# Kernel optimization log

Measured on AMD Instinct MI355X. Metric: run time of the kernel, lower is better.

Reference implementation:

```python
import jax, jax.numpy as jnp
import numpy as np

IN_C, H1, H2, FC1, NCLS = 16, 32, 64, 128, 10
N_NODES, N_EDGES = 20000, 100000


def _glorot(key, shape):
    fan_in, fan_out = shape[0], shape[-1]
    s = jnp.sqrt(6.0 / (fan_in + fan_out))
    return jax.random.uniform(key, shape, jnp.float32, -s, s)


def setup_inputs() -> dict:
    key = jax.random.key(0)
    ks = jax.random.split(key, 20)
    x = jax.random.normal(ks[0], (N_NODES, IN_C), jnp.float32)
    edge_index = jax.random.randint(ks[1], (2, N_EDGES), 0, N_NODES, jnp.int64)
    edge_attr = jax.random.uniform(ks[2], (N_EDGES, 1), jnp.float32)
    return {
        "x": x,
        "edge_index": edge_index,
        "edge_attr": edge_attr,
        # conv1 edge-MLP: 1 -> 25 -> IN_C*H1
        "w1a": _glorot(ks[3], (1, 25)), "b1a": jnp.zeros((25,), jnp.float32),
        "w1b": _glorot(ks[4], (25, IN_C * H1)), "b1b": jnp.zeros((IN_C * H1,), jnp.float32),
        "wr1": _glorot(ks[5], (IN_C, H1)), "bias1": jnp.zeros((H1,), jnp.float32),
        # conv2 edge-MLP: 1 -> 25 -> H1*H2 (=2048)
        "w2a": _glorot(ks[6], (1, 25)), "b2a": jnp.zeros((25,), jnp.float32),
        "w2b": _glorot(ks[7], (25, H1 * H2)), "b2b": jnp.zeros((H1 * H2,), jnp.float32),
        "wr2": _glorot(ks[8], (H1, H2)), "bias2": jnp.zeros((H2,), jnp.float32),
        # trailing FCs
        "fc1_w": _glorot(ks[9], (H2, FC1)), "fc1_b": jnp.zeros((FC1,), jnp.float32),
        "fc2_w": _glorot(ks[10], (FC1, NCLS)), "fc2_b": jnp.zeros((NCLS,), jnp.float32),
    }


def _nnconv(x, src, tgt, edge_attr, wa, ba, wb, bb, wroot, bias, in_c, out_c):
    # per-edge MLP-generated weight matrix [E, in_c, out_c]
    h = jax.nn.relu(edge_attr @ wa + ba) @ wb + bb
    W = h.reshape(-1, in_c, out_c)
    # gather source feats, per-edge matmul, scatter-max to targets
    msg = jnp.einsum("ei,eio->eo", x[src], W)  # [E, out_c]
    agg = jax.ops.segment_max(msg, tgt, num_segments=x.shape[0])
    agg = jnp.where(jnp.isfinite(agg), agg, 0.0)  # nodes with no in-edges -> 0 (PyG behavior)
    return agg + x @ wroot + bias


def reference(x, edge_index, edge_attr,
              w1a, b1a, w1b, b1b, wr1, bias1,
              w2a, b2a, w2b, b2b, wr2, bias2,
              fc1_w, fc1_b, fc2_w, fc2_b):
    src, tgt = edge_index[0], edge_index[1]
    h = jax.nn.elu(_nnconv(x, src, tgt, edge_attr, w1a, b1a, w1b, b1b, wr1, bias1, IN_C, H1))
    h = jax.nn.elu(_nnconv(h, src, tgt, edge_attr, w2a, b2a, w2b, b2b, wr2, bias2, H1, H2))
    h = jax.nn.elu(h @ fc1_w + fc1_b)
    h = h @ fc2_w + fc2_b
    return jax.nn.log_softmax(h, axis=1)
```

## Files before the change

kernel.cpp:

```cpp
#include <hip/hip_runtime.h>
#include <float.h>
#include <math.h>


#define NCONST 25
#define CH1 32
#define CH2 16
#define PACK_MASK 0x1FFFF

__device__ __forceinline__ void atomicMaxFloat(float* addr, float val) {
    if (val >= 0.f) atomicMax((int*)addr, __float_as_int(val));
    else            atomicMin((unsigned int*)addr, __float_as_uint(val));
}
__device__ __forceinline__ float readlane_f(float v, int l) {
    return __int_as_float(__builtin_amdgcn_readlane(__float_as_int(v), l));
}

__global__ void fill_kernel(float* agg, int nAgg, int* ords, int nOrd, int* hist, int nH) {
    int i = blockIdx.x * blockDim.x + threadIdx.x;
    int stride = gridDim.x * blockDim.x;
    int total = nAgg + nOrd + nH;
    for (; i < total; i += stride) {
        if (i < nAgg) agg[i] = -FLT_MAX;
        else if (i < nAgg + nOrd) ords[i - nAgg] = -1;
        else hist[i - nAgg - nOrd] = 0;
    }
}

__global__ void assign_hist_kernel(const float* __restrict__ ea,
                                   const float* __restrict__ w1a, const float* __restrict__ b1a,
                                   const float* __restrict__ w2a, const float* __restrict__ b2a,
                                   int E, int* __restrict__ segpack, int* __restrict__ hist) {
    __shared__ float t1[NCONST], t2[NCONST];
    __shared__ int lh[64];
    int tid = threadIdx.x;
    if (tid < NCONST) {
        float w = w1a[tid]; t1[tid] = (w != 0.f) ? (-b1a[tid] / w) : INFINITY;
        float v = w2a[tid]; t2[tid] = (v != 0.f) ? (-b2a[tid] / v) : INFINITY;
    }
    if (tid < 64) lh[tid] = 0;
    __syncthreads();
    int e = blockIdx.x * blockDim.x + tid;
    bool valid = e < E;
    if (valid) {
        float a = ea[e];
        int j1 = 0, j2 = 0;
        for (int k = 0; k < NCONST; ++k) { j1 += (t1[k] < a); j2 += (t2[k] < a); }
        segpack[e] = j1 | (j2 << 8);
        atomicAdd(&lh[j1], 1); atomicAdd(&lh[32 + j2], 1);
    }
    __syncthreads();
    if (tid < 64 && lh[tid]) atomicAdd(&hist[tid], lh[tid]);
}

__global__ void scanpad_kernel(const int* __restrict__ hist, int* __restrict__ cur) {
    __shared__ int h[64];
    int tid = threadIdx.x;
    h[tid] = hist[tid];
    __syncthreads();
    if (tid == 0) {
        int off = 0;
        for (int j = 0; j < 26; ++j) { cur[j] = off; off += ((h[j] + CH1 - 1) / CH1) * CH1; }
    } else if (tid == 1) {
        int off = 0;
        for (int j = 0; j < 26; ++j) { cur[32 + j] = off; off += ((h[32 + j] + CH2 - 1) / CH2) * CH2; }
    }
}

__global__ void scatter_kernel(const int* __restrict__ segpack, int E, int* __restrict__ cur,
                               int* __restrict__ order1, int* __restrict__ order2) {
    __shared__ int lh[64], lb[64];
    int tid = threadIdx.x;
    if (tid < 64) lh[tid] = 0;
    __syncthreads();
    int e = blockIdx.x * blockDim.x + tid;
    bool valid = e < E;
    int j1 = 0, j2 = 0, r1 = 0, r2 = 0;
    if (valid) {
        int p = segpack[e]; j1 = p & 0xFF; j2 = p >> 8;
        r1 = atomicAdd(&lh[j1], 1); r2 = atomicAdd(&lh[32 + j2], 1);
    }
    __syncthreads();
    if (tid < 64 && lh[tid]) lb[tid] = atomicAdd(&cur[tid], lh[tid]);
    __syncthreads();
    if (valid) {
        order1[lb[j1] + r1] = (j1 << 17) | e;
        order2[lb[32 + j2] + r2] = (j2 << 17) | e;
    }
}

__global__ void build_uv_fused(const float* w1a, const float* b1a, const float* w1b, const float* b1b,
                               const float* w2a, const float* b2a, const float* w2b, const float* b2b,
                               float* U1, float* V1, float* U2, float* V2) {
    __shared__ float swa[NCONST], sba[NCONST], st[NCONST];
    __shared__ int sr[NCONST];
    __shared__ unsigned msk_sh;
    int seg = blockIdx.y;
    int bx = blockIdx.x;
    int conv = (bx < 2) ? 0 : 1;
    const float* wa = conv ? w2a : w1a;
    const float* ba = conv ? b2a : b1a;
    int tid = threadIdx.x;
    if (tid < NCONST) {
        float w = wa[tid], b = ba[tid];
        swa[tid] = w; sba[tid] = b;
        st[tid] = (w != 0.f) ? (-b / w) : INFINITY;
    }
    __syncthreads();
    if (tid < NCONST) {
        int rk = 0;
        for (int l = 0; l < NCONST; ++l) rk += (st[l] < st[tid]) ? 1 : 0;
        sr[tid] = rk;
    }
    __syncthreads();
    if (tid == 0) {
        unsigned m = 0;
        for (int k = 0; k < NCONST; ++k) {
            float w = swa[k];
            bool act = (w > 0.f) ? (seg > sr[k])
                     : (w < 0.f) ? (seg <= sr[k])
                                 : (sba[k] > 0.f);
            if (act) m |= (1u << k);
        }
        msk_sh = m;
    }
    __syncthreads();
    unsigned msk = msk_sh;
    if (conv == 0) {
        int idx = bx * 256 + tid;
        float u = 0.f, v = 0.f;
        for (int k = 0; k < NCONST; ++k)
            if (msk & (1u << k)) { float w = w1b[k * 512 + idx]; u = fmaf(swa[k], w, u); v = fmaf(sba[k], w, v); }
        v += b1b[idx];
        U1[seg * 512 + idx] = u; V1[seg * 512 + idx] = v;
    } else {
        int idx = (bx - 2) * 256 + tid;
        float u = 0.f, v = 0.f;
        for (int k = 0; k < NCONST; ++k)
            if (msk & (1u << k)) { float w = w2b[k * 2048 + idx]; u = fmaf(swa[k], w, u); v = fmaf(sba[k], w, v); }
        v += b2b[idx];
        U2[seg * 2048 + idx] = u; V2[seg * 2048 + idx] = v;
    }
}

__global__ void edge1_kernel(const float* __restrict__ xin, const int* __restrict__ src,
                             const int* __restrict__ tgt, const float* __restrict__ ea,
                             const int* __restrict__ order, int cap,
                             const float* __restrict__ U, const float* __restrict__ V,
                             float* __restrict__ agg) {
    int wid = (blockIdx.x * blockDim.x + threadIdx.x) >> 6;
    int lane = threadIdx.x & 63;
    int base = wid * CH1;
    if (base >= cap) return;
    int pk = order[base + (lane & (CH1 - 1))];
    int p0 = __builtin_amdgcn_readfirstlane(pk);
    if (p0 < 0) return;
    int seg = p0 >> 17;
    int ev = (pk < 0) ? 0 : (pk & PACK_MASK);
    int sv = src[ev], tv = tgt[ev];
    float av = ea[ev];
    int half = lane >> 5, c = lane & 31;
    float Ur[16], Vr[16];
    {
        const float* Us = U + seg * 512 + c;
        const float* Vs = V + seg * 512 + c;
#pragma unroll
        for (int i = 0; i < 16; ++i) { Ur[i] = Us[i * 32]; Vr[i] = Vs[i * 32]; }
    }
#pragma unroll
    for (int t = 0; t < CH1; t += 2) {
        int pA = __builtin_amdgcn_readlane(pk, t);
        int pB = __builtin_amdgcn_readlane(pk, t + 1);
        int sA = __builtin_amdgcn_readlane(sv, t);
        int sB = __builtin_amdgcn_readlane(sv, t + 1);
        int tA = __builtin_amdgcn_readlane(tv, t);
        int tB = __builtin_amdgcn_readlane(tv, t + 1);
        float aA = readlane_f(av, t);
        float aB = readlane_f(av, t + 1);
        const float* xA = xin + sA * 16;
        const float* xB = xin + sB * 16;
        float ah = half ? aB : aA;
        int   th = half ? tB : tA;
        int   ph = half ? pB : pA;
        float acc = 0.f;
#pragma unroll
        for (int i = 0; i < 16; ++i) {
            float xi = half ? xB[i] : xA[i];
            acc = fmaf(xi, fmaf(ah, Ur[i], Vr[i]), acc);
        }
        if (ph >= 0) atomicMaxFloat(&agg[th * 32 + c], acc);
    }
}

__global__ void edge2_kernel(const float* __restrict__ xin, const int* __restrict__ src,
                             const int* __restrict__ tgt, const float* __restrict__ ea,
                             const int* __restrict__ order, int cap,
                             const float* __restrict__ U, const float* __restrict__ V,
                             float* __restrict__ agg) {
    int wid = (blockIdx.x * blockDim.x + threadIdx.x) >> 6;
    int lane = threadIdx.x & 63;
    int base = wid * CH2;
    if (base >= cap) return;
    int pk = order[base + (lane & (CH2 - 1))];
    int p0 = __builtin_amdgcn_readfirstlane(pk);
    if (p0 < 0) return;
    int seg = p0 >> 17;
    int ev = (pk < 0) ? 0 : (pk & PACK_MASK);
    int sv = src[ev], tv = tgt[ev];
    float av = ea[ev];
    float Ur[32], Vr[32];
    {
        const float* Us = U + seg * 2048 + lane;
        const float* Vs = V + seg * 2048 + lane;
#pragma unroll
        for (int i = 0; i < 32; ++i) { Ur[i] = Us[i * 64]; Vr[i] = Vs[i * 64]; }
    }
#pragma unroll
    for (int t = 0; t < CH2; t += 2) {
        int pA = __builtin_amdgcn_readlane(pk, t);
        int pB = __builtin_amdgcn_readlane(pk, t + 1);
        int sA = __builtin_amdgcn_readlane(sv, t);
        int sB = __builtin_amdgcn_readlane(sv, t + 1);
        int tA = __builtin_amdgcn_readlane(tv, t);
        int tB = __builtin_amdgcn_readlane(tv, t + 1);
        float aA = readlane_f(av, t);
        float aB = readlane_f(av, t + 1);
        const float* xA = xin + sA * 32;
        const float* xB = xin + sB * 32;
        float accA = 0.f, accB = 0.f;
#pragma unroll
        for (int i = 0; i < 32; ++i) {
            accA = fmaf(xA[i], fmaf(aA, Ur[i], Vr[i]), accA);
            accB = fmaf(xB[i], fmaf(aB, Ur[i], Vr[i]), accB);
        }
        if (pA >= 0) atomicMaxFloat(&agg[tA * 64 + lane], accA);
        if (pB >= 0) atomicMaxFloat(&agg[tB * 64 + lane], accB);
    }
}

__global__ void node1_kernel(const float* __restrict__ xin, const float* __restrict__ agg,
                             const float* __restrict__ wroot, const float* __restrict__ bias,
                             float* __restrict__ out, int N) {
    int idx = blockIdx.x * blockDim.x + threadIdx.x;
    if (idx >= N * 32) return;
    int n = idx >> 5, c = idx & 31;
    float v = agg[idx];
    if (v == -FLT_MAX) v = 0.f;
    float acc = v + bias[c];
#pragma unroll
    for (int i = 0; i < 16; ++i) acc = fmaf(xin[n * 16 + i], wroot[i * 32 + c], acc);
    out[idx] = acc > 0.f ? acc : expm1f(acc);
}

__global__ void tail_kernel(const float* __restrict__ h1, const float* __restrict__ agg2,
                            const float* __restrict__ wr2, const float* __restrict__ bias2,
                            const float* __restrict__ fc1w, const float* __restrict__ fc1b,
                            const float* __restrict__ fc2w, const float* __restrict__ fc2b,
                            float* __restrict__ out) {
    __shared__ __align__(16) float h2sh[4][64];
    __shared__ __align__(16) float h3sh[4][128];
    int w = threadIdx.x >> 6, lane = threadIdx.x & 63;
    int n = blockIdx.x * 4 + w;
    float v = agg2[n * 64 + lane];
    if (v == -FLT_MAX) v = 0.f;
    float acc = v + bias2[lane];
    const float* xr = h1 + n * 32;
#pragma unroll
    for (int i = 0; i < 32; ++i) acc = fmaf(xr[i], wr2[i * 64 + lane], acc);
    h2sh[w][lane] = acc > 0.f ? acc : expm1f(acc);
    __syncthreads();
    const float4* h2v = (const float4*)h2sh[w];
#pragma unroll
    for (int r = 0; r < 2; ++r) {
        int o = lane + r * 64;
        float a1 = fc1b[o];
#pragma unroll
        for (int q = 0; q < 16; ++q) {
            float4 hv = h2v[q];
            a1 = fmaf(hv.x, fc1w[(q * 4 + 0) * 128 + o], a1);
            a1 = fmaf(hv.y, fc1w[(q * 4 + 1) * 128 + o], a1);
            a1 = fmaf(hv.z, fc1w[(q * 4 + 2) * 128 + o], a1);
            a1 = fmaf(hv.w, fc1w[(q * 4 + 3) * 128 + o], a1);
        }
        h3sh[w][o] = a1 > 0.f ? a1 : expm1f(a1);
    }
    __syncthreads();
    float logit = -FLT_MAX;
    const float4* h3v = (const float4*)h3sh[w];
    if (lane < 10) {
        float a2 = fc2b[lane];
#pragma unroll
        for (int q = 0; q < 32; ++q) {
            float4 hv = h3v[q];
            a2 = fmaf(hv.x, fc2w[(q * 4 + 0) * 10 + lane], a2);
            a2 = fmaf(hv.y, fc2w[(q * 4 + 1) * 10 + lane], a2);
            a2 = fmaf(hv.z, fc2w[(q * 4 + 2) * 10 + lane], a2);
            a2 = fmaf(hv.w, fc2w[(q * 4 + 3) * 10 + lane], a2);
        }
        logit = a2;
    }
    float mx = -FLT_MAX;
#pragma unroll
    for (int i = 0; i < 10; ++i) mx = fmaxf(mx, __shfl(logit, i, 64));
    float s = 0.f;
#pragma unroll
    for (int i = 0; i < 10; ++i) s += expf(__shfl(logit, i, 64) - mx);
    if (lane < 10) out[n * 10 + lane] = logit - mx - logf(s);
}

extern "C" void kernel_launch(void* const* d_in, const int* in_sizes, int n_in,
                              void* d_out, int out_size, void* d_ws, size_t ws_size,
                              hipStream_t stream) {
    const float* x     = (const float*)d_in[0];
    const int*   eidx  = (const int*)d_in[1];
    const float* ea    = (const float*)d_in[2];
    const float* w1a   = (const float*)d_in[3];
    const float* b1a   = (const float*)d_in[4];
    const float* w1b   = (const float*)d_in[5];
    const float* b1b   = (const float*)d_in[6];
    const float* wr1   = (const float*)d_in[7];
    const float* bias1 = (const float*)d_in[8];
    const float* w2a   = (const float*)d_in[9];
    const float* b2a   = (const float*)d_in[10];
    const float* w2b   = (const float*)d_in[11];
    const float* b2b   = (const float*)d_in[12];
    const float* wr2   = (const float*)d_in[13];
    const float* bias2 = (const float*)d_in[14];
    const float* fc1w  = (const float*)d_in[15];
    const float* fc1b  = (const float*)d_in[16];
    const float* fc2w  = (const float*)d_in[17];
    const float* fc2b  = (const float*)d_in[18];

    const int N = in_sizes[0] / 16;
    const int E = in_sizes[2];
    const int* src = eidx;
    const int* tgt = eidx + E;

    const int cap1 = ((E + 26 * (CH1 - 1)) + CH1 - 1) / CH1 * CH1;
    const int cap2 = ((E + 26 * (CH2 - 1)) + CH2 - 1) / CH2 * CH2;

    float* ws = (float*)d_ws;
    size_t off = 0;
    int*      hist = (int*)(ws + off);      off += 64;
    int*      cur  = (int*)(ws + off);      off += 64;
    int*      segp = (int*)(ws + off);      off += E;
    int*      ord1 = (int*)(ws + off);      off += cap1;
    int*      ord2 = (int*)(ws + off);      off += cap2;
    float*    U1   = ws + off;              off += 26 * 512;
    float*    V1   = ws + off;              off += 26 * 512;
    float*    U2   = ws + off;              off += 26 * 2048;
    float*    V2   = ws + off;              off += 26 * 2048;
    float*    AGG1 = ws + off;              off += (size_t)N * 32;
    float*    AGG2 = ws + off;              off += (size_t)N * 64;
    float*    H1b  = ws + off;              off += (size_t)N * 32;

    fill_kernel<<<512, 256, 0, stream>>>(AGG1, N * 96, ord1, cap1 + cap2, hist, 64);
    assign_hist_kernel<<<(E + 255) / 256, 256, 0, stream>>>(ea, w1a, b1a, w2a, b2a, E, segp, hist);
    scanpad_kernel<<<1, 64, 0, stream>>>(hist, cur);
    scatter_kernel<<<(E + 255) / 256, 256, 0, stream>>>(segp, E, cur, ord1, ord2);
    build_uv_fused<<<dim3(10, 26), 256, 0, stream>>>(w1a, b1a, w1b, b1b, w2a, b2a, w2b, b2b,
                                                     U1, V1, U2, V2);
    {
        int waves = cap1 / CH1;
        edge1_kernel<<<(waves + 3) / 4, 256, 0, stream>>>(x, src, tgt, ea, ord1, cap1, U1, V1, AGG1);
    }
    node1_kernel<<<(N * 32 + 255) / 256, 256, 0, stream>>>(x, AGG1, wr1, bias1, H1b, N);
    {
        int waves = cap2 / CH2;
        edge2_kernel<<<(waves + 3) / 4, 256, 0, stream>>>(H1b, src, tgt, ea, ord2, cap2, U2, V2, AGG2);
    }
    tail_kernel<<<N / 4, 256, 0, stream>>>(H1b, AGG2, wr2, bias2, fc1w, fc1b, fc2w, fc2b, (float*)d_out);
}
```

Measured before the change: 231.4 us.

## Process four nodes per wave in tail kernel with register-cached weights

Each wave in the tail kernel now handles four nodes instead of one. The wr2 and fc1 weights are loaded once into registers and reused across those nodes, and fc2 weights are transposed into shared memory. The fc2 and log-softmax step now runs on 16-lane groups covering all four nodes, using xor-shuffle reductions in place of serial shuffles. This cuts repeated global weight loads and idle lanes, at the cost of more registers and a quarter as many blocks.

```diff
diff --git a/kernel.cpp b/kernel.cpp
--- a/kernel.cpp
+++ b/kernel.cpp
@@ -7,6 +7,7 @@
 #define CH1 32
 #define CH2 16
 #define PACK_MASK 0x1FFFF
+#define TNB 4
 
 __device__ __forceinline__ void atomicMaxFloat(float* addr, float val) {
     if (val >= 0.f) atomicMax((int*)addr, __float_as_int(val));
@@ -257,55 +258,107 @@
                             const float* __restrict__ fc1w, const float* __restrict__ fc1b,
                             const float* __restrict__ fc2w, const float* __restrict__ fc2b,
                             float* __restrict__ out) {
-    __shared__ __align__(16) float h2sh[4][64];
-    __shared__ __align__(16) float h3sh[4][128];
-    int w = threadIdx.x >> 6, lane = threadIdx.x & 63;
-    int n = blockIdx.x * 4 + w;
-    float v = agg2[n * 64 + lane];
-    if (v == -FLT_MAX) v = 0.f;
-    float acc = v + bias2[lane];
-    const float* xr = h1 + n * 32;
-#pragma unroll
-    for (int i = 0; i < 32; ++i) acc = fmaf(xr[i], wr2[i * 64 + lane], acc);
-    h2sh[w][lane] = acc > 0.f ? acc : expm1f(acc);
-    __syncthreads();
-    const float4* h2v = (const float4*)h2sh[w];
-#pragma unroll
-    for (int r = 0; r < 2; ++r) {
-        int o = lane + r * 64;
-        float a1 = fc1b[o];
-#pragma unroll
-        for (int q = 0; q < 16; ++q) {
-            float4 hv = h2v[q];
-            a1 = fmaf(hv.x, fc1w[(q * 4 + 0) * 128 + o], a1);
-            a1 = fmaf(hv.y, fc1w[(q * 4 + 1) * 128 + o], a1);
-            a1 = fmaf(hv.z, fc1w[(q * 4 + 2) * 128 + o], a1);
-            a1 = fmaf(hv.w, fc1w[(q * 4 + 3) * 128 + o], a1);
-        }
-        h3sh[w][o] = a1 > 0.f ? a1 : expm1f(a1);
-    }
-    __syncthreads();
-    float logit = -FLT_MAX;
-    const float4* h3v = (const float4*)h3sh[w];
-    if (lane < 10) {
-        float a2 = fc2b[lane];
+    __shared__ __align__(16) float h1sh[4][TNB][32];
+    __shared__ __align__(16) float h2sh[4][TNB][64];
+    __shared__ __align__(16) float h3sh[4][TNB][132];
+    __shared__ __align__(16) float wTsh[10][132];
+    int tid = threadIdx.x;
+    int wv = tid >> 6, lane = tid & 63;
+
+    for (int t = tid; t < 1280; t += 256) {
+        int k = t / 10, j = t - k * 10;
+        wTsh[j][k] = fc2w[t];
+    }
+    __syncthreads();
+
+    int nb = blockIdx.x * (4 * TNB) + wv * TNB;
+
+    {
+        const float2* hp = (const float2*)(h1 + (size_t)nb * 32);
+        ((float2*)&h1sh[wv][0][0])[lane] = hp[lane];
+    }
+
+    float wreg[32];
+#pragma unroll
+    for (int i = 0; i < 32; ++i) wreg[i] = wr2[i * 64 + lane];
+    float b2 = bias2[lane];
+#pragma unroll
+    for (int n = 0; n < TNB; ++n) {
+        float v = agg2[(size_t)(nb + n) * 64 + lane];
+        if (v == -FLT_MAX) v = 0.f;
+        float acc = v + b2;
+        const float4* hv = (const float4*)h1sh[wv][n];
+#pragma unroll
+        for (int q = 0; q < 8; ++q) {
+            float4 h = hv[q];
+            acc = fmaf(h.x, wreg[q * 4 + 0], acc);
+            acc = fmaf(h.y, wreg[q * 4 + 1], acc);
+            acc = fmaf(h.z, wreg[q * 4 + 2], acc);
+            acc = fmaf(h.w, wreg[q * 4 + 3], acc);
+        }
+        h2sh[wv][n][lane] = acc > 0.f ? acc : expm1f(acc);
+    }
+
+    float acc1[TNB], acc2[TNB];
+    {
+        float fb1 = fc1b[lane], fb2 = fc1b[64 + lane];
+#pragma unroll
+        for (int n = 0; n < TNB; ++n) { acc1[n] = fb1; acc2[n] = fb2; }
+    }
+#pragma unroll
+    for (int q = 0; q < 16; ++q) {
+        float wa0 = fc1w[(q * 4 + 0) * 128 + lane];
+        float wb0 = fc1w[(q * 4 + 0) * 128 + 64 + lane];
+        float wa1 = fc1w[(q * 4 + 1) * 128 + lane];
+        float wb1 = fc1w[(q * 4 + 1) * 128 + 64 + lane];
+        float wa2 = fc1w[(q * 4 + 2) * 128 + lane];
+        float wb2 = fc1w[(q * 4 + 2) * 128 + 64 + lane];
+        float wa3 = fc1w[(q * 4 + 3) * 128 + lane];
+        float wb3 = fc1w[(q * 4 + 3) * 128 + 64 + lane];
+#pragma unroll
+        for (int n = 0; n < TNB; ++n) {
+            float4 h = ((const float4*)h2sh[wv][n])[q];
+            acc1[n] = fmaf(h.x, wa0, acc1[n]); acc2[n] = fmaf(h.x, wb0, acc2[n]);
+            acc1[n] = fmaf(h.y, wa1, acc1[n]); acc2[n] = fmaf(h.y, wb1, acc2[n]);
+            acc1[n] = fmaf(h.z, wa2, acc1[n]); acc2[n] = fmaf(h.z, wb2, acc2[n]);
+            acc1[n] = fmaf(h.w, wa3, acc1[n]); acc2[n] = fmaf(h.w, wb3, acc2[n]);
+        }
+    }
+#pragma unroll
+    for (int n = 0; n < TNB; ++n) {
+        float a = acc1[n], b = acc2[n];
+        h3sh[wv][n][lane]      = a > 0.f ? a : expm1f(a);
+        h3sh[wv][n][64 + lane] = b > 0.f ? b : expm1f(b);
+    }
+
+    {
+        int n = lane >> 4, j = lane & 15;
+        bool act = j < 10;
+        int jc = act ? j : 0;
+        float a = fc2b[jc];
+        const float4* h3v = (const float4*)h3sh[wv][n];
+        const float4* wv4 = (const float4*)wTsh[jc];
 #pragma unroll
         for (int q = 0; q < 32; ++q) {
-            float4 hv = h3v[q];
-            a2 = fmaf(hv.x, fc2w[(q * 4 + 0) * 10 + lane], a2);
-            a2 = fmaf(hv.y, fc2w[(q * 4 + 1) * 10 + lane], a2);
-            a2 = fmaf(hv.z, fc2w[(q * 4 + 2) * 10 + lane], a2);
-            a2 = fmaf(hv.w, fc2w[(q * 4 + 3) * 10 + lane], a2);
-        }
-        logit = a2;
-    }
-    float mx = -FLT_MAX;
-#pragma unroll
-    for (int i = 0; i < 10; ++i) mx = fmaxf(mx, __shfl(logit, i, 64));
-    float s = 0.f;
-#pragma unroll
-    for (int i = 0; i < 10; ++i) s += expf(__shfl(logit, i, 64) - mx);
-    if (lane < 10) out[n * 10 + lane] = logit - mx - logf(s);
+            float4 h = h3v[q];
+            float4 w = wv4[q];
+            a = fmaf(h.x, w.x, a);
+            a = fmaf(h.y, w.y, a);
+            a = fmaf(h.z, w.z, a);
+            a = fmaf(h.w, w.w, a);
+        }
+        float lm = act ? a : -FLT_MAX;
+        lm = fmaxf(lm, __shfl_xor(lm, 1, 16));
+        lm = fmaxf(lm, __shfl_xor(lm, 2, 16));
+        lm = fmaxf(lm, __shfl_xor(lm, 4, 16));
+        lm = fmaxf(lm, __shfl_xor(lm, 8, 16));
+        float ls = act ? expf(a - lm) : 0.f;
+        ls += __shfl_xor(ls, 1, 16);
+        ls += __shfl_xor(ls, 2, 16);
+        ls += __shfl_xor(ls, 4, 16);
+        ls += __shfl_xor(ls, 8, 16);
+        if (act) out[(size_t)(nb + n) * 10 + j] = a - lm - logf(ls);
+    }
 }
 
 extern "C" void kernel_launch(void* const* d_in, const int* in_sizes, int n_in,
@@ -369,5 +422,5 @@
         int waves = cap2 / CH2;
         edge2_kernel<<<(waves + 3) / 4, 256, 0, stream>>>(H1b, src, tgt, ea, ord2, cap2, U2, V2, AGG2);
     }
-    tail_kernel<<<N / 4, 256, 0, stream>>>(H1b, AGG2, wr2, bias2, fc1w, fc1b, fc2w, fc2b, (float*)d_out);
-}
+    tail_kernel<<<N / 16, 256, 0, stream>>>(H1b, AGG2, wr2, bias2, fc1w, fc1b, fc2w, fc2b, (float*)d_out);
+}
```

After: 479.2 us. 2.07x slower.
